# Kernel tuning notes

Hardware: AMD Instinct MI355X
Metric: run time of the kernel (lower is better)

Reference implementation:

```python
import jax, jax.numpy as jnp
import numpy as np

V = 50257   # vocab size
E = 256     # embedding_dimension
D = 8       # key_query_reduced_dimensionality
H = 8       # no_of_attention_heads
L = 16      # no_of_blocks
B = 8       # batch
T = 512     # seq len == context_size
FF = 4 * E  # MLP hidden


def setup_inputs() -> dict:
    key = jax.random.key(0)
    ks = jax.random.split(key, 12)
    rn = lambda k, s: jax.random.normal(k, s, jnp.float32) * 0.02
    return {
        'tokens': jax.random.randint(ks[0], (B, T), 0, V),
        'ideal_value': jax.random.randint(ks[1], (B, T), 0, V),
        'tok_emb': rn(ks[2], (V, E)),
        'pos_emb': rn(ks[3], (T, E)),
        'Wq': rn(ks[4], (L, H, E, D)),
        'Wk': rn(ks[5], (L, H, E, D)),
        'Wv': rn(ks[6], (L, H, E, D)),
        'Wo': rn(ks[7], (L, H * D, E)),
        'bo': jnp.zeros((L, E), jnp.float32),
        'ln1_s': jnp.ones((L, E), jnp.float32),
        'ln1_b': jnp.zeros((L, E), jnp.float32),
        'W1': rn(ks[8], (L, E, FF)),
        'b1': jnp.zeros((L, FF), jnp.float32),
        'W2': rn(ks[9], (L, FF, E)),
        'b2': jnp.zeros((L, E), jnp.float32),
        'ln2_s': jnp.ones((L, E), jnp.float32),
        'ln2_b': jnp.zeros((L, E), jnp.float32),
        'lnf_s': jnp.ones((E,), jnp.float32),
        'lnf_b': jnp.zeros((E,), jnp.float32),
        'Wf': rn(ks[10], (E, V)),
        'bf': jnp.zeros((V,), jnp.float32),
    }


def _ln(x, s, b):
    m = x.mean(-1, keepdims=True)
    v = ((x - m) ** 2).mean(-1, keepdims=True)
    return (x - m) * jax.lax.rsqrt(v + 1e-5) * s + b


def reference(tokens, ideal_value, tok_emb, pos_emb, Wq, Wk, Wv, Wo, bo,
              ln1_s, ln1_b, W1, b1, W2, b2, ln2_s, ln2_b, lnf_s, lnf_b, Wf, bf):
    Bn, Tn = tokens.shape
    x = tok_emb[tokens] + pos_emb[:Tn]                      # [B,T,E]
    # faithful mask: masked_fill where transpose(tril(R))==0 -> keep upper triangle
    keep = jnp.triu(jnp.ones((D, D), bool))
    scale = jnp.float32(E) ** 0.5

    def block(x, p):
        wq, wk, wv, wo, bo_, s1, bb1, w1, bm1, w2, bm2, s2, bb2 = p
        h = _ln(x, s1, bb1)
        Q = jnp.einsum('bte,hed->bhtd', h, wq)              # [B,H,T,D]
        K = jnp.einsum('bte,hed->bhtd', h, wk)
        Vv = jnp.einsum('bte,hed->bhtd', h, wv)
        # R = K^T @ Q : feature-by-feature [B,H,D,D] (this repo's quirky attention)
        R = jnp.einsum('bhti,bhtj->bhij', K, Q) / scale
        R = jax.nn.softmax(jnp.where(keep, R, -jnp.inf), axis=-1)
        a = jnp.einsum('bhti,bhij->bhtj', Vv, R)            # V @ R, [B,H,T,D]
        a = a.transpose(0, 2, 1, 3).reshape(x.shape[0], x.shape[1], H * D)
        x = x + a @ wo + bo_                                # dropout is identity (eval)
        h2 = _ln(x, s2, bb2)
        x = x + jax.nn.relu(h2 @ w1 + bm1) @ w2 + bm2
        return x, None

    x, _ = jax.lax.scan(block, x, (Wq, Wk, Wv, Wo, bo, ln1_s, ln1_b,
                                   W1, b1, W2, b2, ln2_s, ln2_b))
    logits = (_ln(x, lnf_s, lnf_b) @ Wf + bf).reshape(-1, V)  # [B*T, V]
    tgt = ideal_value.reshape(-1)
    logp = jax.nn.log_softmax(logits, axis=-1)
    loss = -jnp.take_along_axis(logp, tgt[:, None], axis=1).mean()
    return logits, loss
```

## Files before the change

kernel.cpp:

```cpp
#include <hip/hip_runtime.h>
#include <math.h>

#define V_SZ 50257
#define NPAD 50432
#define NCB 197

#define AS1 __attribute__((address_space(1)))
#define AS3 __attribute__((address_space(3)))

typedef short s16x8 __attribute__((ext_vector_type(8)));
typedef ushort u16x4 __attribute__((ext_vector_type(4)));
typedef float f32x4 __attribute__((ext_vector_type(4)));

__device__ __forceinline__ ushort f2bf(float x) {
    union { float f; unsigned u; } v; v.f = x;
    unsigned r = v.u + 0x7FFF + ((v.u >> 16) & 1);
    return (ushort)(r >> 16);
}
__device__ __forceinline__ float bf2f(ushort u) {
    union { unsigned u; float f; } v; v.u = ((unsigned)u) << 16; return v.f;
}

__global__ __launch_bounds__(256) void gpt_embed_ln(const int* __restrict__ tokens,
                                                    const float* __restrict__ tok_emb,
                                                    const float* __restrict__ pos_emb,
                                                    const float* __restrict__ s, const float* __restrict__ b,
                                                    float* __restrict__ x, ushort* __restrict__ hb) {
    int wave = threadIdx.x >> 6, lane = threadIdx.x & 63;
    int row = blockIdx.x * 4 + wave;
    int t = row & 511;
    int tok = tokens[row];
    float4 te = ((const float4*)(tok_emb + tok * 256))[lane];
    float4 pe = ((const float4*)(pos_emb + t * 256))[lane];
    float4 v = make_float4(te.x + pe.x, te.y + pe.y, te.z + pe.z, te.w + pe.w);
    ((float4*)(x + row * 256))[lane] = v;
    float sum = v.x + v.y + v.z + v.w;
    #pragma unroll
    for (int off = 1; off < 64; off <<= 1) sum += __shfl_xor(sum, off);
    float mean = sum * (1.0f / 256.0f);
    float dx = v.x - mean, dy = v.y - mean, dz = v.z - mean, dw = v.w - mean;
    float vs = dx * dx + dy * dy + dz * dz + dw * dw;
    #pragma unroll
    for (int off = 1; off < 64; off <<= 1) vs += __shfl_xor(vs, off);
    float rstd = rsqrtf(vs * (1.0f / 256.0f) + 1e-5f);
    float4 sv = ((const float4*)s)[lane];
    float4 bv = ((const float4*)b)[lane];
    u16x4 o;
    o[0] = f2bf(dx * rstd * sv.x + bv.x);
    o[1] = f2bf(dy * rstd * sv.y + bv.y);
    o[2] = f2bf(dz * rstd * sv.z + bv.z);
    o[3] = f2bf(dw * rstd * sv.w + bv.w);
    *(u16x4*)&hb[row * 256 + lane * 4] = o;
}

__global__ __launch_bounds__(256) void cvt_transpose(const float* __restrict__ in, ushort* __restrict__ out,
                                                     int Kd, int Nd, int n_real,
                                                     int in_stride, int out_stride) {
    __shared__ __align__(16) ushort t[64][80];
    const float* inp = in + (size_t)blockIdx.z * in_stride;
    ushort* outp = out + (size_t)blockIdx.z * out_stride;
    int n0 = blockIdx.x * 64, k0 = blockIdx.y * 64;
    int tid = threadIdx.x;
    #pragma unroll
    for (int p = 0; p < 4; p++) {
        int lk = p * 16 + (tid >> 4);
        int ln = (tid & 15) * 4;
        int k = k0 + lk, n = n0 + ln;
        const float* rowp = inp + (size_t)k * Nd;
        float v0 = 0.f, v1 = 0.f, v2 = 0.f, v3 = 0.f;
        if (n + 0 < n_real) v0 = rowp[n + 0];
        if (n + 1 < n_real) v1 = rowp[n + 1];
        if (n + 2 < n_real) v2 = rowp[n + 2];
        if (n + 3 < n_real) v3 = rowp[n + 3];
        t[ln + 0][lk] = f2bf(v0);
        t[ln + 1][lk] = f2bf(v1);
        t[ln + 2][lk] = f2bf(v2);
        t[ln + 3][lk] = f2bf(v3);
    }
    __syncthreads();
    int ln = tid >> 2, kq = (tid & 3) * 16;
    ushort* op = outp + (size_t)(n0 + ln) * Kd + k0 + kq;
    *(s16x8*)&op[0] = *(const s16x8*)&t[ln][kq];
    *(s16x8*)&op[8] = *(const s16x8*)&t[ln][kq + 8];
}

__global__ __launch_bounds__(256) void cvt_qkv(const float* __restrict__ Wq, const float* __restrict__ Wk,
                                               const float* __restrict__ Wv, ushort* __restrict__ WqkvT) {
    int l = blockIdx.x, kind = blockIdx.y;
    const float* W = (kind == 0 ? Wq : (kind == 1 ? Wk : Wv)) + l * 16384;
    ushort* out = WqkvT + (size_t)l * 65536 + kind * 64 * 256;
    int tid = threadIdx.x;
    #pragma unroll 4
    for (int it = 0; it < 64; it++) {
        int idx = it * 256 + tid;
        int row = idx >> 8, e = idx & 255;
        int h = row >> 3, d = row & 7;
        out[row * 256 + e] = f2bf(W[h * 2048 + e * 8 + d]);
    }
    if (kind == 0) {
        ushort* zp = WqkvT + (size_t)l * 65536 + 192 * 256;
        #pragma unroll 4
        for (int it = 0; it < 64; it++) zp[it * 256 + tid] = 0;
    }
}

__global__ __launch_bounds__(512, 4) void gpt_pre(const ushort* __restrict__ hb,
                                                  const ushort* __restrict__ WqkvT,
                                                  ushort* __restrict__ Vb,
                                                  float* __restrict__ Rpart) {
    __shared__ __align__(16) ushort As[16 * 64];
    __shared__ __align__(16) ushort Bs[256 * 64];
    __shared__ float kqv[16][193];
    const int tid = threadIdx.x, lane = tid & 63, wn = tid >> 6;
    const int rows0 = blockIdx.x * 16;
    const int fr = lane & 15, fkb = (lane >> 4) * 16;
    const int arow = tid >> 3, ach = tid & 7;

    f32x4 acc[2];
    acc[0] = (f32x4)0.0f; acc[1] = (f32x4)0.0f;

    s16x8 ra, rb[4];
    if (tid < 128) ra = *(const s16x8*)&hb[(size_t)(rows0 + arow) * 256 + ach * 8];
    #pragma unroll
    for (int i = 0; i < 4; i++) {
        int u = tid + i * 512, r = u >> 3, ch = u & 7;
        rb[i] = *(const s16x8*)&WqkvT[(size_t)r * 256 + ch * 8];
    }
    #pragma unroll 1
    for (int kt = 0; kt < 4; kt++) {
        if (kt) __syncthreads();
        if (tid < 128)
            *(s16x8*)&As[arow * 64 + (((ach * 16) ^ ((arow & 7) << 4)) >> 1)] = ra;
        #pragma unroll
        for (int i = 0; i < 4; i++) {
            int u = tid + i * 512, r = u >> 3, ch = u & 7;
            *(s16x8*)&Bs[r * 64 + (((ch * 16) ^ ((r & 7) << 4)) >> 1)] = rb[i];
        }
        __syncthreads();
        if (kt < 3) {
            int k0 = (kt + 1) * 64;
            if (tid < 128) ra = *(const s16x8*)&hb[(size_t)(rows0 + arow) * 256 + k0 + ach * 8];
            #pragma unroll
            for (int i = 0; i < 4; i++) {
                int u = tid + i * 512, r = u >> 3, ch = u & 7;
                rb[i] = *(const s16x8*)&WqkvT[(size_t)r * 256 + k0 + ch * 8];
            }
        }
        #pragma unroll
        for (int kk = 0; kk < 2; kk++) {
            int kbyte = kk * 64 + fkb;
            s16x8 af = *(const s16x8*)&As[fr * 64 + ((kbyte ^ ((fr & 7) << 4)) >> 1)];
            #pragma unroll
            for (int n = 0; n < 2; n++) {
                int brow = wn * 32 + n * 16 + fr;
                s16x8 bfv = *(const s16x8*)&Bs[brow * 64 + ((kbyte ^ ((brow & 7) << 4)) >> 1)];
                acc[n] = __builtin_amdgcn_mfma_f32_16x16x32_bf16(af, bfv, acc[n], 0, 0, 0);
            }
        }
    }
    #pragma unroll
    for (int n = 0; n < 2; n++) {
        int col = wn * 32 + n * 16 + fr;
        if (col < 192) {
            #pragma unroll
            for (int r = 0; r < 4; r++)
                kqv[(lane >> 4) * 4 + r][col] = acc[n][r];
        }
    }
    __syncthreads();
    #pragma unroll
    for (int i = 0; i < 2; i++) {
        int u = tid + i * 512, t = u >> 6, hd = u & 63;
        Vb[(size_t)(rows0 + t) * 64 + hd] = f2bf(kqv[t][128 + hd]);
    }
    {
        int h = tid >> 6, i2 = (tid >> 3) & 7, j = tid & 7;
        float s = 0.0f;
        #pragma unroll
        for (int t = 0; t < 16; t++)
            s += kqv[t][64 + h * 8 + i2] * kqv[t][h * 8 + j];
        int bb = rows0 >> 9, part = (rows0 >> 4) & 31;
        Rpart[(size_t)(bb * 32 + part) * 512 + tid] = s;
    }
}

__global__ __launch_bounds__(512, 4) void gpt_layer(
        const float* __restrict__ Rpart_in, const ushort* __restrict__ Vb_in,
        const ushort* __restrict__ WoT, const float* __restrict__ bo,
        const ushort* __restrict__ W1T, const float* __restrict__ b1,
        const ushort* __restrict__ W2T, const float* __restrict__ b2,
        const float* __restrict__ ls2, const float* __restrict__ lb2,
        const float* __restrict__ nls, const float* __restrict__ nlb,
        float* __restrict__ x,
        const ushort* __restrict__ WqkvT_next,
        ushort* __restrict__ Vb_out, float* __restrict__ Rpart_out,
        ushort* __restrict__ hbout, int mode) {
    __shared__ __align__(16) ushort Bs[256 * 64];
    __shared__ __align__(16) ushort ffs[16 * 1024];
    __shared__ __align__(16) ushort h2s[16 * 256];
    __shared__ __align__(16) ushort abl[16 * 64];
    __shared__ __align__(16) ushort Vl[16 * 64];
    __shared__ float Rs[512];
    __shared__ float red1[16][8], red2[16][8], mrow[16], rrow[16];

    const int tid = threadIdx.x, lane = tid & 63, wn = tid >> 6;
    const int rows0 = blockIdx.x * 16, b = rows0 >> 9;
    const int fr = lane & 15, fkb = (lane >> 4) * 16, rbase = (lane >> 4) * 4;
    int colv[2]; colv[0] = wn * 32 + fr; colv[1] = wn * 32 + 16 + fr;
    int srow_[4], sch_[4];
    #pragma unroll
    for (int i = 0; i < 4; i++) {
        int u = lane + i * 64;
        srow_[i] = wn * 32 + (u >> 3);
        sch_[i] = u & 7;
    }

    float xr[2][4];
    #pragma unroll
    for (int n = 0; n < 2; n++)
        #pragma unroll
        for (int r = 0; r < 4; r++)
            xr[n][r] = x[(size_t)(rows0 + rbase + r) * 256 + colv[n]];

    {
        const float* rp = Rpart_in + (size_t)b * 32 * 512 + tid;
        float s = 0.0f;
        #pragma unroll
        for (int p = 0; p < 32; p++) s += rp[p * 512];
        s *= (1.0f / 16.0f);
        int ii = (tid >> 3) & 7, j = tid & 7;
        float val = (j >= ii) ? s : -INFINITY;
        float m = val;
        #pragma unroll
        for (int off = 1; off < 8; off <<= 1) m = fmaxf(m, __shfl_xor(m, off, 8));
        float ex = __expf(val - m);
        float su = ex;
        #pragma unroll
        for (int off = 1; off < 8; off <<= 1) su += __shfl_xor(su, off, 8);
        Rs[tid] = ex / su;
    }
    #pragma unroll
    for (int i = 0; i < 2; i++) {
        int u = tid + i * 512, t = u >> 6, hd = u & 63;
        Vl[t * 64 + hd] = Vb_in[(size_t)(rows0 + t) * 64 + hd];
    }
    __syncthreads();
    #pragma unroll
    for (int i = 0; i < 2; i++) {
        int u = tid + i * 512, t = u >> 6, hd = u & 63, h = hd >> 3, j = hd & 7;
        float a = 0.0f;
        #pragma unroll
        for (int q = 0; q < 8; q++)
            a += bf2f(Vl[t * 64 + h * 8 + q]) * Rs[h * 64 + q * 8 + j];
        abl[t * 64 + (((hd * 2) ^ ((t & 7) << 4)) >> 1)] = f2bf(a);
    }
    s16x8 rbv[4];
    #pragma unroll
    for (int i = 0; i < 4; i++)
        rbv[i] = *(const s16x8*)&WoT[(size_t)srow_[i] * 64 + sch_[i] * 8];
    __syncthreads();
    #pragma unroll
    for (int i = 0; i < 4; i++)
        *(s16x8*)&Bs[srow_[i] * 64 + (((sch_[i] * 16) ^ ((srow_[i] & 7) << 4)) >> 1)] = rbv[i];
    f32x4 acc[2];
    acc[0] = (f32x4)0.0f; acc[1] = (f32x4)0.0f;
    __builtin_amdgcn_s_setprio(1);
    #pragma unroll
    for (int kk = 0; kk < 2; kk++) {
        int kbyte = kk * 64 + fkb;
        s16x8 af = *(const s16x8*)&abl[fr * 64 + ((kbyte ^ ((fr & 7) << 4)) >> 1)];
        #pragma unroll
        for (int n = 0; n < 2; n++) {
            int brow = wn * 32 + n * 16 + fr;
            s16x8 bfv = *(const s16x8*)&Bs[brow * 64 + ((kbyte ^ ((brow & 7) << 4)) >> 1)];
            acc[n] = __builtin_amdgcn_mfma_f32_16x16x32_bf16(af, bfv, acc[n], 0, 0, 0);
        }
    }
    __builtin_amdgcn_s_setprio(0);
    float xn[2][4];
    #pragma unroll
    for (int n = 0; n < 2; n++) {
        int col = colv[n];
        float bbv = bo[col];
        #pragma unroll
        for (int r = 0; r < 4; r++)
            xn[n][r] = acc[n][r] + bbv + xr[n][r];
    }
    #pragma unroll
    for (int r = 0; r < 4; r++) {
        float s1 = xn[0][r] + xn[1][r];
        float s2 = xn[0][r] * xn[0][r] + xn[1][r] * xn[1][r];
        #pragma unroll
        for (int off = 1; off < 16; off <<= 1) {
            s1 += __shfl_xor(s1, off);
            s2 += __shfl_xor(s2, off);
        }
        if (fr == 0) { red1[rbase + r][wn] = s1; red2[rbase + r][wn] = s2; }
    }
    __syncthreads();
    if (tid < 16) {
        float s1 = 0.f, s2 = 0.f;
        #pragma unroll
        for (int w = 0; w < 8; w++) { s1 += red1[tid][w]; s2 += red2[tid][w]; }
        float mean = s1 * (1.0f / 256.0f);
        float var = s2 * (1.0f / 256.0f) - mean * mean;
        mrow[tid] = mean;
        rrow[tid] = rsqrtf(var + 1e-5f);
    }
    __syncthreads();
    #pragma unroll
    for (int n = 0; n < 2; n++) {
        int col = colv[n];
        float lsv = ls2[col], lbv = lb2[col];
        #pragma unroll
        for (int r = 0; r < 4; r++) {
            int rl = rbase + r;
            float hv = (xn[n][r] - mrow[rl]) * rrow[rl] * lsv + lbv;
            h2s[rl * 256 + (((col * 2) ^ ((rl & 7) << 4)) >> 1)] = f2bf(hv);
        }
    }
    __syncthreads();
    #pragma unroll 1
    for (int c = 0; c < 4; c++) {
        const ushort* Bg = W1T + (size_t)c * 256 * 256;
        acc[0] = (f32x4)0.0f; acc[1] = (f32x4)0.0f;
        #pragma unroll
        for (int i = 0; i < 4; i++)
            rbv[i] = *(const s16x8*)&Bg[(size_t)srow_[i] * 256 + sch_[i] * 8];
        #pragma unroll 1
        for (int kt = 0; kt < 4; kt++) {
            #pragma unroll
            for (int i = 0; i < 4; i++)
                *(s16x8*)&Bs[srow_[i] * 64 + (((sch_[i] * 16) ^ ((srow_[i] & 7) << 4)) >> 1)] = rbv[i];
            if (kt < 3) {
                int k0 = (kt + 1) * 64;
                #pragma unroll
                for (int i = 0; i < 4; i++)
                    rbv[i] = *(const s16x8*)&Bg[(size_t)srow_[i] * 256 + k0 + sch_[i] * 8];
            }
            __builtin_amdgcn_s_setprio(1);
            #pragma unroll
            for (int kk = 0; kk < 2; kk++) {
                int kbyte = kt * 128 + kk * 64 + fkb;
                s16x8 af = *(const s16x8*)&h2s[fr * 256 + ((kbyte ^ ((fr & 7) << 4)) >> 1)];
                int kb2 = kk * 64 + fkb;
                #pragma unroll
                for (int n = 0; n < 2; n++) {
                    int brow = wn * 32 + n * 16 + fr;
                    s16x8 bfv = *(const s16x8*)&Bs[brow * 64 + ((kb2 ^ ((brow & 7) << 4)) >> 1)];
                    acc[n] = __builtin_amdgcn_mfma_f32_16x16x32_bf16(af, bfv, acc[n], 0, 0, 0);
                }
            }
            __builtin_amdgcn_s_setprio(0);
        }
        #pragma unroll
        for (int n = 0; n < 2; n++) {
            int col = c * 256 + colv[n];
            float bb1 = b1[col];
            #pragma unroll
            for (int r = 0; r < 4; r++) {
                int rl = rbase + r;
                ffs[rl * 1024 + (((col * 2) ^ ((rl & 7) << 4)) >> 1)] =
                    f2bf(fmaxf(acc[n][r] + bb1, 0.0f));
            }
        }
    }
    __syncthreads();
    f32x4 a2[2];
    a2[0] = (f32x4)0.0f; a2[1] = (f32x4)0.0f;
    #pragma unroll
    for (int i = 0; i < 4; i++)
        rbv[i] = *(const s16x8*)&W2T[(size_t)srow_[i] * 1024 + sch_[i] * 8];
    #pragma unroll 2
    for (int kt = 0; kt < 16; kt++) {
        #pragma unroll
        for (int i = 0; i < 4; i++)
            *(s16x8*)&Bs[srow_[i] * 64 + (((sch_[i] * 16) ^ ((srow_[i] & 7) << 4)) >> 1)] = rbv[i];
        if (kt < 15) {
            int k0 = (kt + 1) * 64;
            #pragma unroll
            for (int i = 0; i < 4; i++)
                rbv[i] = *(const s16x8*)&W2T[(size_t)srow_[i] * 1024 + k0 + sch_[i] * 8];
        }
        __builtin_amdgcn_s_setprio(1);
        #pragma unroll
        for (int kk = 0; kk < 2; kk++) {
            int kbyte = kt * 128 + kk * 64 + fkb;
            s16x8 af = *(const s16x8*)&ffs[fr * 1024 + ((kbyte ^ ((fr & 7) << 4)) >> 1)];
            int kb2 = kk * 64 + fkb;
            #pragma unroll
            for (int n = 0; n < 2; n++) {
                int brow = wn * 32 + n * 16 + fr;
                s16x8 bfv = *(const s16x8*)&Bs[brow * 64 + ((kb2 ^ ((brow & 7) << 4)) >> 1)];
                a2[n] = __builtin_amdgcn_mfma_f32_16x16x32_bf16(af, bfv, a2[n], 0, 0, 0);
            }
        }
        __builtin_amdgcn_s_setprio(0);
    }
    #pragma unroll
    for (int n = 0; n < 2; n++) {
        int col = colv[n];
        float bb2 = b2[col];
        #pragma unroll
        for (int r = 0; r < 4; r++) {
            float v = xn[n][r] + a2[n][r] + bb2;
            xn[n][r] = v;
            x[(size_t)(rows0 + rbase + r) * 256 + col] = v;
        }
    }
    __syncthreads();
    #pragma unroll
    for (int r = 0; r < 4; r++) {
        float s1 = xn[0][r] + xn[1][r];
        float s2 = xn[0][r] * xn[0][r] + xn[1][r] * xn[1][r];
        #pragma unroll
        for (int off = 1; off < 16; off <<= 1) {
            s1 += __shfl_xor(s1, off);
            s2 += __shfl_xor(s2, off);
        }
        if (fr == 0) { red1[rbase + r][wn] = s1; red2[rbase + r][wn] = s2; }
    }
    __syncthreads();
    if (tid < 16) {
        float s1 = 0.f, s2 = 0.f;
        #pragma unroll
        for (int w = 0; w < 8; w++) { s1 += red1[tid][w]; s2 += red2[tid][w]; }
        float mean = s1 * (1.0f / 256.0f);
        float var = s2 * (1.0f / 256.0f) - mean * mean;
        mrow[tid] = mean;
        rrow[tid] = rsqrtf(var + 1e-5f);
    }
    __syncthreads();
    #pragma unroll
    for (int n = 0; n < 2; n++) {
        int col = colv[n];
        float lsv = nls[col], lbv = nlb[col];
        #pragma unroll
        for (int r = 0; r < 4; r++) {
            int rl = rbase + r;
            float hv = (xn[n][r] - mrow[rl]) * rrow[rl] * lsv + lbv;
            ushort hu = f2bf(hv);
            h2s[rl * 256 + (((col * 2) ^ ((rl & 7) << 4)) >> 1)] = hu;
            if (mode == 0)
                hbout[(size_t)(rows0 + rl) * 256 + col] = hu;
        }
    }
    if (mode == 0) return;
    __syncthreads();

    float* kqv = (float*)ffs;
    acc[0] = (f32x4)0.0f; acc[1] = (f32x4)0.0f;
    #pragma unroll
    for (int i = 0; i < 4; i++)
        rbv[i] = *(const s16x8*)&WqkvT_next[(size_t)srow_[i] * 256 + sch_[i] * 8];
    #pragma unroll 1
    for (int kt = 0; kt < 4; kt++) {
        #pragma unroll
        for (int i = 0; i < 4; i++)
            *(s16x8*)&Bs[srow_[i] * 64 + (((sch_[i] * 16) ^ ((srow_[i] & 7) << 4)) >> 1)] = rbv[i];
        if (kt < 3) {
            int k0 = (kt + 1) * 64;
            #pragma unroll
            for (int i = 0; i < 4; i++)
                rbv[i] = *(const s16x8*)&WqkvT_next[(size_t)srow_[i] * 256 + k0 + sch_[i] * 8];
        }
        __builtin_amdgcn_s_setprio(1);
        #pragma unroll
        for (int kk = 0; kk < 2; kk++) {
            int kbyte = kt * 128 + kk * 64 + fkb;
            s16x8 af = *(const s16x8*)&h2s[fr * 256 + ((kbyte ^ ((fr & 7) << 4)) >> 1)];
            int kb2 = kk * 64 + fkb;
            #pragma unroll
            for (int n = 0; n < 2; n++) {
                int brow = wn * 32 + n * 16 + fr;
                s16x8 bfv = *(const s16x8*)&Bs[brow * 64 + ((kb2 ^ ((brow & 7) << 4)) >> 1)];
                acc[n] = __builtin_amdgcn_mfma_f32_16x16x32_bf16(af, bfv, acc[n], 0, 0, 0);
            }
        }
        __builtin_amdgcn_s_setprio(0);
    }
    __syncthreads();
    #pragma unroll
    for (int n = 0; n < 2; n++) {
        int col = wn * 32 + n * 16 + fr;
        if (col < 192) {
            #pragma unroll
            for (int r = 0; r < 4; r++)
                kqv[(rbase + r) * 193 + col] = acc[n][r];
        }
    }
    __syncthreads();
    #pragma unroll
    for (int i = 0; i < 2; i++) {
        int u = tid + i * 512, t = u >> 6, hd = u & 63;
        Vb_out[(size_t)(rows0 + t) * 64 + hd] = f2bf(kqv[t * 193 + 128 + hd]);
    }
    {
        int h = tid >> 6, i2 = (tid >> 3) & 7, j = tid & 7;
        float s = 0.0f;
        #pragma unroll
        for (int t = 0; t < 16; t++)
            s += kqv[t * 193 + 64 + h * 8 + i2] * kqv[t * 193 + h * 8 + j];
        int part = (rows0 >> 4) & 31;
        Rpart_out[(size_t)(b * 32 + part) * 512 + tid] = s;
    }
}

__global__ __launch_bounds__(512, 4) void gpt_logits_mfma(const ushort* __restrict__ hb, const ushort* __restrict__ WfT,
                                                          const float* __restrict__ bfb, float* __restrict__ out,
                                                          float2* __restrict__ lsebuf) {
    __shared__ __align__(16) ushort As[128 * 64];
    __shared__ __align__(16) ushort Bs[256 * 64];
    f32x4 acc[4][4];
    int flat = blockIdx.y * 32 + blockIdx.x;
    int nf = (flat & 7) * 788 + (flat >> 3);
    int rb = nf & 31, cb = nf >> 5;
    int row0 = rb * 128, c0 = cb * 256;
    const int tid = threadIdx.x, lane = tid & 63, wid = tid >> 6;
    const int wm = wid >> 2, wn = wid & 3;
    const int fr = lane & 15, fkb = (lane >> 4) * 16;

    #pragma unroll
    for (int m = 0; m < 4; m++)
        #pragma unroll
        for (int n = 0; n < 4; n++) acc[m][n] = (f32x4)0.0f;

    float bb[4]; int gcv[4];
    #pragma unroll
    for (int n = 0; n < 4; n++) {
        int gc = c0 + wn * 64 + n * 16 + fr;
        gcv[n] = gc;
        bb[n] = (gc < V_SZ) ? bfb[gc] : 0.0f;
    }

    const int srow = lane >> 3;
    const int sch = lane & 7;
    #pragma unroll 1
    for (int kt = 0; kt < 4; kt++) {
        if (kt) __syncthreads();
        {
            int kb = kt * 64;
            #pragma unroll
            for (int i = 0; i < 2; i++) {
                int rloc = wid * 16 + i * 8 + srow;
                int cs = sch ^ (rloc & 7);
                const ushort* gp = &hb[(size_t)(row0 + rloc) * 256 + kb + cs * 8];
                __builtin_amdgcn_global_load_lds((const AS1 void*)gp,
                                                 (AS3 void*)&As[(wid * 16 + i * 8) * 64], 16, 0, 0);
            }
            #pragma unroll
            for (int i = 0; i < 4; i++) {
                int rloc = wid * 32 + i * 8 + srow;
                int cs = sch ^ (rloc & 7);
                const ushort* gp = &WfT[(size_t)(c0 + rloc) * 256 + kb + cs * 8];
                __builtin_amdgcn_global_load_lds((const AS1 void*)gp,
                                                 (AS3 void*)&Bs[(wid * 32 + i * 8) * 64], 16, 0, 0);
            }
        }
        __syncthreads();
        #pragma unroll
        for (int kk = 0; kk < 2; kk++) {
            int kbyte = kk * 64 + fkb;
            s16x8 af[4], bfr[4];
            #pragma unroll
            for (int m = 0; m < 4; m++) {
                int arow = wm * 64 + m * 16 + fr;
                af[m] = *(const s16x8*)&As[arow * 64 + ((kbyte ^ ((arow & 7) << 4)) >> 1)];
            }
            #pragma unroll
            for (int n = 0; n < 4; n++) {
                int brow = wn * 64 + n * 16 + fr;
                bfr[n] = *(const s16x8*)&Bs[brow * 64 + ((kbyte ^ ((brow & 7) << 4)) >> 1)];
            }
            #pragma unroll
            for (int m = 0; m < 4; m++)
                #pragma unroll
                for (int n = 0; n < 4; n++)
                    acc[m][n] = __builtin_amdgcn_mfma_f32_16x16x32_bf16(af[m], bfr[n], acc[m][n], 0, 0, 0);
        }
    }
    __syncthreads();
    float2 (*red)[4] = (float2(*)[4])As;
    #pragma unroll
    for (int m = 0; m < 4; m++) {
        int rloc = wm * 64 + m * 16 + (lane >> 4) * 4;
        int gr = row0 + rloc;
        #pragma unroll
// ... 302 lines not shown
            acc1[r] += hv.x * w10 + hv.y * w11 + hv.z * w12 + hv.w * w13;
        }
    }
    if (c0 < V_SZ) {
        #pragma unroll
        for (int r = 0; r < 32; r++) out[(size_t)(row0 + r) * V_SZ + c0] = acc0[r];
    }
    if (c1 < V_SZ) {
        #pragma unroll
        for (int r = 0; r < 32; r++) out[(size_t)(row0 + r) * V_SZ + c1] = acc1[r];
    }
}

__global__ void gpt_loss(const float* __restrict__ logits, const int* __restrict__ tgt,
                         float* __restrict__ partial) {
    __shared__ float ms[256], ss[256];
    int row = blockIdx.x, tid = threadIdx.x;
    const float* lr = logits + (size_t)row * V_SZ;
    float m = -INFINITY, s = 0.0f;
    for (int c = tid; c < V_SZ; c += 256) {
        float v = lr[c];
        float nm = fmaxf(m, v);
        s = s * expf(m - nm) + expf(v - nm);
        m = nm;
    }
    ms[tid] = m; ss[tid] = s;
    __syncthreads();
    for (int off = 128; off > 0; off >>= 1) {
        if (tid < off) {
            float m2 = ms[tid + off], s2 = ss[tid + off];
            float M = fmaxf(ms[tid], m2);
            ss[tid] = ss[tid] * expf(ms[tid] - M) + s2 * expf(m2 - M);
            ms[tid] = M;
        }
        __syncthreads();
    }
    if (tid == 0) {
        float lse = ms[0] + logf(ss[0]);
        partial[row] = lse - lr[tgt[row]];
    }
}

extern "C" void kernel_launch(void* const* d_in, const int* in_sizes, int n_in,
                              void* d_out, int out_size, void* d_ws, size_t ws_size,
                              hipStream_t stream) {
    const int*   tokens  = (const int*)d_in[0];
    const int*   ideal   = (const int*)d_in[1];
    const float* tok_emb = (const float*)d_in[2];
    const float* pos_emb = (const float*)d_in[3];
    const float* Wq      = (const float*)d_in[4];
    const float* Wk      = (const float*)d_in[5];
    const float* Wv      = (const float*)d_in[6];
    const float* Wo      = (const float*)d_in[7];
    const float* bo      = (const float*)d_in[8];
    const float* ln1_s   = (const float*)d_in[9];
    const float* ln1_b   = (const float*)d_in[10];
    const float* W1      = (const float*)d_in[11];
    const float* b1      = (const float*)d_in[12];
    const float* W2      = (const float*)d_in[13];
    const float* b2      = (const float*)d_in[14];
    const float* ln2_s   = (const float*)d_in[15];
    const float* ln2_b   = (const float*)d_in[16];
    const float* lnf_s   = (const float*)d_in[17];
    const float* lnf_b   = (const float*)d_in[18];
    const float* Wf      = (const float*)d_in[19];
    const float* bf      = (const float*)d_in[20];
    float* out = (float*)d_out;

    size_t off = 0;
    char* wsc = (char*)d_ws;
    ushort* WfT   = (ushort*)(wsc + off); off += (size_t)NPAD * 256 * 2;
    ushort* W1T   = (ushort*)(wsc + off); off += (size_t)16 * 1024 * 256 * 2;
    ushort* W2T   = (ushort*)(wsc + off); off += (size_t)16 * 256 * 1024 * 2;
    ushort* WqkvT = (ushort*)(wsc + off); off += (size_t)16 * 256 * 256 * 2;
    ushort* WoT   = (ushort*)(wsc + off); off += (size_t)16 * 256 * 64 * 2;
    ushort* hb    = (ushort*)(wsc + off); off += (size_t)4096 * 256 * 2;
    ushort* Vb0   = (ushort*)(wsc + off); off += (size_t)4096 * 64 * 2;
    ushort* Vb1   = (ushort*)(wsc + off); off += (size_t)4096 * 64 * 2;
    float*  x     = (float*)(wsc + off);  off += (size_t)4096 * 256 * 4;
    float*  Rp0   = (float*)(wsc + off);  off += (size_t)8 * 32 * 512 * 4;
    float*  Rp1   = (float*)(wsc + off);  off += (size_t)8 * 32 * 512 * 4;
    float*  partial = (float*)(wsc + off); off += (size_t)4096 * 4;
    float2* lsebuf = (float2*)(wsc + off); off += (size_t)4096 * NCB * 8;
    bool big = ws_size >= off;

    if (big) {
        cvt_transpose<<<dim3(16, 4, 16), 256, 0, stream>>>(W1, W1T, 256, 1024, 1024, 262144, 262144);
        cvt_transpose<<<dim3(4, 16, 16), 256, 0, stream>>>(W2, W2T, 1024, 256, 256, 262144, 262144);
        cvt_transpose<<<dim3(4, 1, 16), 256, 0, stream>>>(Wo, WoT, 64, 256, 256, 16384, 16384);
        cvt_transpose<<<dim3(788, 4, 1), 256, 0, stream>>>(Wf, WfT, 256, V_SZ, V_SZ, 0, 0);
        cvt_qkv<<<dim3(16, 3), 256, 0, stream>>>(Wq, Wk, Wv, WqkvT);

        gpt_embed_ln<<<1024, 256, 0, stream>>>(tokens, tok_emb, pos_emb, ln1_s, ln1_b, x, hb);
        gpt_pre<<<256, 512, 0, stream>>>(hb, WqkvT, Vb0, Rp0);

        for (int l = 0; l < 16; l++) {
            const float* nls = (l < 15) ? ln1_s + (l + 1) * 256 : lnf_s;
            const float* nlb = (l < 15) ? ln1_b + (l + 1) * 256 : lnf_b;
            const float* Rin = (l & 1) ? Rp1 : Rp0;
            const ushort* Vin = (l & 1) ? Vb1 : Vb0;
            float* Rout = (l & 1) ? Rp0 : Rp1;
            ushort* Vout = (l & 1) ? Vb0 : Vb1;
            int mode = (l < 15) ? 1 : 0;
            const ushort* Wnext = WqkvT + (size_t)((l < 15) ? (l + 1) : 0) * 65536;
            gpt_layer<<<256, 512, 0, stream>>>(Rin, Vin,
                                               WoT + (size_t)l * 16384, bo + l * 256,
                                               W1T + (size_t)l * 262144, b1 + l * 1024,
                                               W2T + (size_t)l * 262144, b2 + l * 256,
                                               ln2_s + l * 256, ln2_b + l * 256,
                                               nls, nlb, x,
                                               Wnext, Vout, Rout, hb, mode);
        }

        gpt_logits_mfma<<<dim3(32, NCB), 512, 0, stream>>>(hb, WfT, bf, out, lsebuf);
        gpt_lse<<<1024, 256, 0, stream>>>(lsebuf, out, ideal, partial);
        gpt_loss_reduce<<<1, 256, 0, stream>>>(partial, out + (size_t)4096 * V_SZ);
    } else {
        float* fx  = (float*)d_ws;
        float* fh  = fx + 4096 * 256;
        float* fQ  = fh + 4096 * 256;
        float* fK  = fQ + 4096 * 64;
        float* fV  = fK + 4096 * 64;
        float* fR  = fV + 4096 * 64;
        float* fpart = fR + 64 * 64;
        gpt_embed<<<4096, 256, 0, stream>>>(tokens, tok_emb, pos_emb, fx);
        for (int l = 0; l < 16; l++) {
            gpt_ln<<<4096, 256, 0, stream>>>(fx, ln1_s + l * 256, ln1_b + l * 256, fh);
            gpt_qkv<<<512, 256, 0, stream>>>(fh, Wq + l * 16384, Wk + l * 16384, Wv + l * 16384, fQ, fK, fV);
            gpt_attn_r<<<64, 64, 0, stream>>>(fK, fQ, fR);
            gpt_attn_out<<<512, 256, 0, stream>>>(fV, fR, Wo + l * 16384, bo + l * 256, fx);
            gpt_ln<<<4096, 256, 0, stream>>>(fx, ln2_s + l * 256, ln2_b + l * 256, fh);
            gpt_mlp<<<512, 256, 0, stream>>>(fh, W1 + l * 262144, b1 + l * 1024, W2 + l * 262144, b2 + l * 256, fx);
        }
        gpt_ln<<<4096, 256, 0, stream>>>(fx, lnf_s, lnf_b, fh);
        dim3 lg(99, 128);
        gpt_logits<<<lg, 256, 0, stream>>>(fh, Wf, bf, out);
        gpt_loss<<<4096, 256, 0, stream>>>(out, ideal, fpart);
        gpt_loss_reduce<<<1, 256, 0, stream>>>(fpart, out + (size_t)4096 * V_SZ);
    }
}
```

Before: 910.0 us.

## Fuse all transformer layers into one persistent kernel with grid barriers

Replaces the sixteen per-layer launches with one persistent kernel that loops over layers. Each 16-row block keeps its residual stream in registers instead of reloading and storing x every layer. Layers are separated by a global atomic-counter barrier, since the attention R reduction needs every block of a batch. This removes launch gaps and global traffic for x. The cost is a spin-wait barrier, which relies on all 256 blocks being resident at once.

```diff
diff --git a/kernel.cpp b/kernel.cpp
--- a/kernel.cpp
+++ b/kernel.cpp
@@ -19,6 +19,10 @@
 }
 __device__ __forceinline__ float bf2f(ushort u) {
     union { unsigned u; float f; } v; v.u = ((unsigned)u) << 16; return v.f;
+}
+
+__global__ void gpt_zero(unsigned* __restrict__ c) {
+    if (threadIdx.x < 16) c[threadIdx.x] = 0;
 }
 
 __global__ __launch_bounds__(256) void gpt_embed_ln(const int* __restrict__ tokens,
@@ -184,17 +188,18 @@
     }
 }
 
-__global__ __launch_bounds__(512, 4) void gpt_layer(
-        const float* __restrict__ Rpart_in, const ushort* __restrict__ Vb_in,
-        const ushort* __restrict__ WoT, const float* __restrict__ bo,
-        const ushort* __restrict__ W1T, const float* __restrict__ b1,
-        const ushort* __restrict__ W2T, const float* __restrict__ b2,
-        const float* __restrict__ ls2, const float* __restrict__ lb2,
-        const float* __restrict__ nls, const float* __restrict__ nlb,
-        float* __restrict__ x,
-        const ushort* __restrict__ WqkvT_next,
-        ushort* __restrict__ Vb_out, float* __restrict__ Rpart_out,
-        ushort* __restrict__ hbout, int mode) {
+__global__ __launch_bounds__(512, 4) void gpt_layers_all(
+        float* __restrict__ Rp0, ushort* __restrict__ Vb0,
+        float* __restrict__ Rp1, ushort* __restrict__ Vb1,
+        const ushort* __restrict__ WoT_a, const float* __restrict__ bo_a,
+        const ushort* __restrict__ W1T_a, const float* __restrict__ b1_a,
+        const ushort* __restrict__ W2T_a, const float* __restrict__ b2_a,
+        const float* __restrict__ ln2s_a, const float* __restrict__ ln2b_a,
+        const float* __restrict__ ln1s_a, const float* __restrict__ ln1b_a,
+        const float* __restrict__ lnf_s, const float* __restrict__ lnf_b,
+        const ushort* __restrict__ WqkvT_a,
+        const float* __restrict__ x0, ushort* __restrict__ hbout,
+        unsigned* __restrict__ cnts) {
     __shared__ __align__(16) ushort Bs[256 * 64];
     __shared__ __align__(16) ushort ffs[16 * 1024];
     __shared__ __align__(16) ushort h2s[16 * 256];
@@ -215,118 +220,258 @@
         sch_[i] = u & 7;
     }
 
-    float xr[2][4];
+    float xc[2][4];
     #pragma unroll
     for (int n = 0; n < 2; n++)
         #pragma unroll
         for (int r = 0; r < 4; r++)
-            xr[n][r] = x[(size_t)(rows0 + rbase + r) * 256 + colv[n]];
-
-    {
-        const float* rp = Rpart_in + (size_t)b * 32 * 512 + tid;
-        float s = 0.0f;
-        #pragma unroll
-        for (int p = 0; p < 32; p++) s += rp[p * 512];
-        s *= (1.0f / 16.0f);
-        int ii = (tid >> 3) & 7, j = tid & 7;
-        float val = (j >= ii) ? s : -INFINITY;
-        float m = val;
-        #pragma unroll
-        for (int off = 1; off < 8; off <<= 1) m = fmaxf(m, __shfl_xor(m, off, 8));
-        float ex = __expf(val - m);
-        float su = ex;
-        #pragma unroll
-        for (int off = 1; off < 8; off <<= 1) su += __shfl_xor(su, off, 8);
-        Rs[tid] = ex / su;
-    }
-    #pragma unroll
-    for (int i = 0; i < 2; i++) {
-        int u = tid + i * 512, t = u >> 6, hd = u & 63;
-        Vl[t * 64 + hd] = Vb_in[(size_t)(rows0 + t) * 64 + hd];
-    }
-    __syncthreads();
-    #pragma unroll
-    for (int i = 0; i < 2; i++) {
-        int u = tid + i * 512, t = u >> 6, hd = u & 63, h = hd >> 3, j = hd & 7;
-        float a = 0.0f;
-        #pragma unroll
-        for (int q = 0; q < 8; q++)
-            a += bf2f(Vl[t * 64 + h * 8 + q]) * Rs[h * 64 + q * 8 + j];
-        abl[t * 64 + (((hd * 2) ^ ((t & 7) << 4)) >> 1)] = f2bf(a);
-    }
-    s16x8 rbv[4];
-    #pragma unroll
-    for (int i = 0; i < 4; i++)
-        rbv[i] = *(const s16x8*)&WoT[(size_t)srow_[i] * 64 + sch_[i] * 8];
-    __syncthreads();
-    #pragma unroll
-    for (int i = 0; i < 4; i++)
-        *(s16x8*)&Bs[srow_[i] * 64 + (((sch_[i] * 16) ^ ((srow_[i] & 7) << 4)) >> 1)] = rbv[i];
-    f32x4 acc[2];
-    acc[0] = (f32x4)0.0f; acc[1] = (f32x4)0.0f;
-    __builtin_amdgcn_s_setprio(1);
-    #pragma unroll
-    for (int kk = 0; kk < 2; kk++) {
-        int kbyte = kk * 64 + fkb;
-        s16x8 af = *(const s16x8*)&abl[fr * 64 + ((kbyte ^ ((fr & 7) << 4)) >> 1)];
+            xc[n][r] = x0[(size_t)(rows0 + rbase + r) * 256 + colv[n]];
+
+    #pragma unroll 1
+    for (int l = 0; l < 16; l++) {
+        const float*  Rpart_in  = (l & 1) ? Rp1 : Rp0;
+        const ushort* Vb_in     = (l & 1) ? Vb1 : Vb0;
+        float*        Rpart_out = (l & 1) ? Rp0 : Rp1;
+        ushort*       Vb_out    = (l & 1) ? Vb0 : Vb1;
+        const ushort* WoT = WoT_a + (size_t)l * 16384;
+        const float*  bo  = bo_a + l * 256;
+        const ushort* W1T = W1T_a + (size_t)l * 262144;
+        const float*  b1  = b1_a + l * 1024;
+        const ushort* W2T = W2T_a + (size_t)l * 262144;
+        const float*  b2  = b2_a + l * 256;
+        const float*  ls2 = ln2s_a + l * 256;
+        const float*  lb2 = ln2b_a + l * 256;
+        const int mode = (l < 15);
+        const float* nls = mode ? ln1s_a + (l + 1) * 256 : lnf_s;
+        const float* nlb = mode ? ln1b_a + (l + 1) * 256 : lnf_b;
+        const ushort* WqkvT_next = WqkvT_a + (size_t)(mode ? (l + 1) : 0) * 65536;
+
+        {
+            const float* rp = Rpart_in + (size_t)b * 32 * 512 + tid;
+            float s = 0.0f;
+            #pragma unroll
+            for (int p = 0; p < 32; p++) s += rp[p * 512];
+            s *= (1.0f / 16.0f);
+            int ii = (tid >> 3) & 7, j = tid & 7;
+            float val = (j >= ii) ? s : -INFINITY;
+            float m = val;
+            #pragma unroll
+            for (int off = 1; off < 8; off <<= 1) m = fmaxf(m, __shfl_xor(m, off, 8));
+            float ex = __expf(val - m);
+            float su = ex;
+            #pragma unroll
+            for (int off = 1; off < 8; off <<= 1) su += __shfl_xor(su, off, 8);
+            Rs[tid] = ex / su;
+        }
+        #pragma unroll
+        for (int i = 0; i < 2; i++) {
+            int u = tid + i * 512, t = u >> 6, hd = u & 63;
+            Vl[t * 64 + hd] = Vb_in[(size_t)(rows0 + t) * 64 + hd];
+        }
+        __syncthreads();
+        #pragma unroll
+        for (int i = 0; i < 2; i++) {
+            int u = tid + i * 512, t = u >> 6, hd = u & 63, h = hd >> 3, j = hd & 7;
+            float a = 0.0f;
+            #pragma unroll
+            for (int q = 0; q < 8; q++)
+                a += bf2f(Vl[t * 64 + h * 8 + q]) * Rs[h * 64 + q * 8 + j];
+            abl[t * 64 + (((hd * 2) ^ ((t & 7) << 4)) >> 1)] = f2bf(a);
+        }
+        s16x8 rbv[4];
+        #pragma unroll
+        for (int i = 0; i < 4; i++)
+            rbv[i] = *(const s16x8*)&WoT[(size_t)srow_[i] * 64 + sch_[i] * 8];
+        __syncthreads();
+        #pragma unroll
+        for (int i = 0; i < 4; i++)
+            *(s16x8*)&Bs[srow_[i] * 64 + (((sch_[i] * 16) ^ ((srow_[i] & 7) << 4)) >> 1)] = rbv[i];
+        f32x4 acc[2];
+        acc[0] = (f32x4)0.0f; acc[1] = (f32x4)0.0f;
+        __builtin_amdgcn_s_setprio(1);
+        #pragma unroll
+        for (int kk = 0; kk < 2; kk++) {
+            int kbyte = kk * 64 + fkb;
+            s16x8 af = *(const s16x8*)&abl[fr * 64 + ((kbyte ^ ((fr & 7) << 4)) >> 1)];
+            #pragma unroll
+            for (int n = 0; n < 2; n++) {
+                int brow = wn * 32 + n * 16 + fr;
+                s16x8 bfv = *(const s16x8*)&Bs[brow * 64 + ((kbyte ^ ((brow & 7) << 4)) >> 1)];
+                acc[n] = __builtin_amdgcn_mfma_f32_16x16x32_bf16(af, bfv, acc[n], 0, 0, 0);
+            }
+        }
+        __builtin_amdgcn_s_setprio(0);
+        float xn[2][4];
         #pragma unroll
         for (int n = 0; n < 2; n++) {
-            int brow = wn * 32 + n * 16 + fr;
-            s16x8 bfv = *(const s16x8*)&Bs[brow * 64 + ((kbyte ^ ((brow & 7) << 4)) >> 1)];
-            acc[n] = __builtin_amdgcn_mfma_f32_16x16x32_bf16(af, bfv, acc[n], 0, 0, 0);
-        }
-    }
-    __builtin_amdgcn_s_setprio(0);
-    float xn[2][4];
-    #pragma unroll
-    for (int n = 0; n < 2; n++) {
-        int col = colv[n];
-        float bbv = bo[col];
-        #pragma unroll
-        for (int r = 0; r < 4; r++)
-            xn[n][r] = acc[n][r] + bbv + xr[n][r];
-    }
-    #pragma unroll
-    for (int r = 0; r < 4; r++) {
-        float s1 = xn[0][r] + xn[1][r];
-        float s2 = xn[0][r] * xn[0][r] + xn[1][r] * xn[1][r];
-        #pragma unroll
-        for (int off = 1; off < 16; off <<= 1) {
-            s1 += __shfl_xor(s1, off);
-            s2 += __shfl_xor(s2, off);
-        }
-        if (fr == 0) { red1[rbase + r][wn] = s1; red2[rbase + r][wn] = s2; }
-    }
-    __syncthreads();
-    if (tid < 16) {
-        float s1 = 0.f, s2 = 0.f;
-        #pragma unroll
-        for (int w = 0; w < 8; w++) { s1 += red1[tid][w]; s2 += red2[tid][w]; }
-        float mean = s1 * (1.0f / 256.0f);
-        float var = s2 * (1.0f / 256.0f) - mean * mean;
-        mrow[tid] = mean;
-        rrow[tid] = rsqrtf(var + 1e-5f);
-    }
-    __syncthreads();
-    #pragma unroll
-    for (int n = 0; n < 2; n++) {
-        int col = colv[n];
-        float lsv = ls2[col], lbv = lb2[col];
+            float bbv = bo[colv[n]];
+            #pragma unroll
+            for (int r = 0; r < 4; r++)
+                xn[n][r] = acc[n][r] + bbv + xc[n][r];
+        }
         #pragma unroll
         for (int r = 0; r < 4; r++) {
-            int rl = rbase + r;
-            float hv = (xn[n][r] - mrow[rl]) * rrow[rl] * lsv + lbv;
-            h2s[rl * 256 + (((col * 2) ^ ((rl & 7) << 4)) >> 1)] = f2bf(hv);
-        }
-    }
-    __syncthreads();
-    #pragma unroll 1
-    for (int c = 0; c < 4; c++) {
-        const ushort* Bg = W1T + (size_t)c * 256 * 256;
+            float s1 = xn[0][r] + xn[1][r];
+            float s2 = xn[0][r] * xn[0][r] + xn[1][r] * xn[1][r];
+            #pragma unroll
+            for (int off = 1; off < 16; off <<= 1) {
+                s1 += __shfl_xor(s1, off);
+                s2 += __shfl_xor(s2, off);
+            }
+            if (fr == 0) { red1[rbase + r][wn] = s1; red2[rbase + r][wn] = s2; }
+        }
+        __syncthreads();
+        if (tid < 16) {
+            float s1 = 0.f, s2 = 0.f;
+            #pragma unroll
+            for (int w = 0; w < 8; w++) { s1 += red1[tid][w]; s2 += red2[tid][w]; }
+            float mean = s1 * (1.0f / 256.0f);
+            float var = s2 * (1.0f / 256.0f) - mean * mean;
+            mrow[tid] = mean;
+            rrow[tid] = rsqrtf(var + 1e-5f);
+        }
+        __syncthreads();
+        #pragma unroll
+        for (int n = 0; n < 2; n++) {
+            int col = colv[n];
+            float lsv = ls2[col], lbv = lb2[col];
+            #pragma unroll
+            for (int r = 0; r < 4; r++) {
+                int rl = rbase + r;
+                float hv = (xn[n][r] - mrow[rl]) * rrow[rl] * lsv + lbv;
+                h2s[rl * 256 + (((col * 2) ^ ((rl & 7) << 4)) >> 1)] = f2bf(hv);
+            }
+        }
+        __syncthreads();
+        #pragma unroll 1
+        for (int c = 0; c < 4; c++) {
+            const ushort* Bg = W1T + (size_t)c * 256 * 256;
+            acc[0] = (f32x4)0.0f; acc[1] = (f32x4)0.0f;
+            #pragma unroll
+            for (int i = 0; i < 4; i++)
+                rbv[i] = *(const s16x8*)&Bg[(size_t)srow_[i] * 256 + sch_[i] * 8];
+            #pragma unroll 1
+            for (int kt = 0; kt < 4; kt++) {
+                #pragma unroll
+                for (int i = 0; i < 4; i++)
+                    *(s16x8*)&Bs[srow_[i] * 64 + (((sch_[i] * 16) ^ ((srow_[i] & 7) << 4)) >> 1)] = rbv[i];
+                if (kt < 3) {
+                    int k0 = (kt + 1) * 64;
+                    #pragma unroll
+                    for (int i = 0; i < 4; i++)
+                        rbv[i] = *(const s16x8*)&Bg[(size_t)srow_[i] * 256 + k0 + sch_[i] * 8];
+                }
+                __builtin_amdgcn_s_setprio(1);
+                #pragma unroll
+                for (int kk = 0; kk < 2; kk++) {
+                    int kbyte = kt * 128 + kk * 64 + fkb;
+                    s16x8 af = *(const s16x8*)&h2s[fr * 256 + ((kbyte ^ ((fr & 7) << 4)) >> 1)];
+                    int kb2 = kk * 64 + fkb;
+                    #pragma unroll
+                    for (int n = 0; n < 2; n++) {
+                        int brow = wn * 32 + n * 16 + fr;
+                        s16x8 bfv = *(const s16x8*)&Bs[brow * 64 + ((kb2 ^ ((brow & 7) << 4)) >> 1)];
+                        acc[n] = __builtin_amdgcn_mfma_f32_16x16x32_bf16(af, bfv, acc[n], 0, 0, 0);
+                    }
+                }
+                __builtin_amdgcn_s_setprio(0);
+            }
+            #pragma unroll
+            for (int n = 0; n < 2; n++) {
+                int col = c * 256 + colv[n];
+                float bb1 = b1[col];
+                #pragma unroll
+                for (int r = 0; r < 4; r++) {
+                    int rl = rbase + r;
+                    ffs[rl * 1024 + (((col * 2) ^ ((rl & 7) << 4)) >> 1)] =
+                        f2bf(fmaxf(acc[n][r] + bb1, 0.0f));
+                }
+            }
+        }
+        __syncthreads();
+        f32x4 a2[2];
+        a2[0] = (f32x4)0.0f; a2[1] = (f32x4)0.0f;
+        #pragma unroll
+        for (int i = 0; i < 4; i++)
+            rbv[i] = *(const s16x8*)&W2T[(size_t)srow_[i] * 1024 + sch_[i] * 8];
+        #pragma unroll 2
+        for (int kt = 0; kt < 16; kt++) {
+            #pragma unroll
+            for (int i = 0; i < 4; i++)
+                *(s16x8*)&Bs[srow_[i] * 64 + (((sch_[i] * 16) ^ ((srow_[i] & 7) << 4)) >> 1)] = rbv[i];
+            if (kt < 15) {
+                int k0 = (kt + 1) * 64;
+                #pragma unroll
+                for (int i = 0; i < 4; i++)
+                    rbv[i] = *(const s16x8*)&W2T[(size_t)srow_[i] * 1024 + k0 + sch_[i] * 8];
+            }
+            __builtin_amdgcn_s_setprio(1);
+            #pragma unroll
+            for (int kk = 0; kk < 2; kk++) {
+                int kbyte = kt * 128 + kk * 64 + fkb;
+                s16x8 af = *(const s16x8*)&ffs[fr * 1024 + ((kbyte ^ ((fr & 7) << 4)) >> 1)];
+                int kb2 = kk * 64 + fkb;
+                #pragma unroll
+                for (int n = 0; n < 2; n++) {
+                    int brow = wn * 32 + n * 16 + fr;
+                    s16x8 bfv = *(const s16x8*)&Bs[brow * 64 + ((kb2 ^ ((brow & 7) << 4)) >> 1)];
+                    a2[n] = __builtin_amdgcn_mfma_f32_16x16x32_bf16(af, bfv, a2[n], 0, 0, 0);
+                }
+            }
+            __builtin_amdgcn_s_setprio(0);
+        }
+        #pragma unroll
+        for (int n = 0; n < 2; n++) {
+            float bb2 = b2[colv[n]];
+            #pragma unroll
+            for (int r = 0; r < 4; r++)
+                xc[n][r] = xn[n][r] + a2[n][r] + bb2;
+        }
+        __syncthreads();
+        #pragma unroll
+        for (int r = 0; r < 4; r++) {
+            float s1 = xc[0][r] + xc[1][r];
+            float s2 = xc[0][r] * xc[0][r] + xc[1][r] * xc[1][r];
+            #pragma unroll
+            for (int off = 1; off < 16; off <<= 1) {
+                s1 += __shfl_xor(s1, off);
+                s2 += __shfl_xor(s2, off);
+            }
+            if (fr == 0) { red1[rbase + r][wn] = s1; red2[rbase + r][wn] = s2; }
+        }
+        __syncthreads();
+        if (tid < 16) {
+            float s1 = 0.f, s2 = 0.f;
+            #pragma unroll
+            for (int w = 0; w < 8; w++) { s1 += red1[tid][w]; s2 += red2[tid][w]; }
+            float mean = s1 * (1.0f / 256.0f);
+            float var = s2 * (1.0f / 256.0f) - mean * mean;
+            mrow[tid] = mean;
+            rrow[tid] = rsqrtf(var + 1e-5f);
+        }
+        __syncthreads();
+        #pragma unroll
+        for (int n = 0; n < 2; n++) {
+            int col = colv[n];
+            float lsv = nls[col], lbv = nlb[col];
+            #pragma unroll
+            for (int r = 0; r < 4; r++) {
+                int rl = rbase + r;
+                float hv = (xc[n][r] - mrow[rl]) * rrow[rl] * lsv + lbv;
+                ushort hu = f2bf(hv);
+                h2s[rl * 256 + (((col * 2) ^ ((rl & 7) << 4)) >> 1)] = hu;
+                if (!mode)
+                    hbout[(size_t)(rows0 + rl) * 256 + col] = hu;
+            }
+        }
+        if (!mode) break;
+        __syncthreads();
+
+        float* kqv = (float*)ffs;
         acc[0] = (f32x4)0.0f; acc[1] = (f32x4)0.0f;
         #pragma unroll
         for (int i = 0; i < 4; i++)
-            rbv[i] = *(const s16x8*)&Bg[(size_t)srow_[i] * 256 + sch_[i] * 8];
+            rbv[i] = *(const s16x8*)&WqkvT_next[(size_t)srow_[i] * 256 + sch_[i] * 8];
         #pragma unroll 1
         for (int kt = 0; kt < 4; kt++) {
             #pragma unroll
@@ -336,7 +481,7 @@
                 int k0 = (kt + 1) * 64;
                 #pragma unroll
                 for (int i = 0; i < 4; i++)
-                    rbv[i] = *(const s16x8*)&Bg[(size_t)srow_[i] * 256 + k0 + sch_[i] * 8];
+                    rbv[i] = *(const s16x8*)&WqkvT_next[(size_t)srow_[i] * 256 + k0 + sch_[i] * 8];
             }
             __builtin_amdgcn_s_setprio(1);
             #pragma unroll
@@ -353,156 +498,40 @@
             }
             __builtin_amdgcn_s_setprio(0);
         }
+        __syncthreads();
         #pragma unroll
         for (int n = 0; n < 2; n++) {
-            int col = c * 256 + colv[n];
-            float bb1 = b1[col];
-            #pragma unroll
-            for (int r = 0; r < 4; r++) {
-                int rl = rbase + r;
-                ffs[rl * 1024 + (((col * 2) ^ ((rl & 7) << 4)) >> 1)] =
-                    f2bf(fmaxf(acc[n][r] + bb1, 0.0f));
-            }
-        }
-    }
-    __syncthreads();
-    f32x4 a2[2];
-    a2[0] = (f32x4)0.0f; a2[1] = (f32x4)0.0f;
-    #pragma unroll
-    for (int i = 0; i < 4; i++)
-        rbv[i] = *(const s16x8*)&W2T[(size_t)srow_[i] * 1024 + sch_[i] * 8];
-    #pragma unroll 2
-    for (int kt = 0; kt < 16; kt++) {
-        #pragma unroll
-        for (int i = 0; i < 4; i++)
-            *(s16x8*)&Bs[srow_[i] * 64 + (((sch_[i] * 16) ^ ((srow_[i] & 7) << 4)) >> 1)] = rbv[i];
-        if (kt < 15) {
-            int k0 = (kt + 1) * 64;
-            #pragma unroll
-            for (int i = 0; i < 4; i++)
-                rbv[i] = *(const s16x8*)&W2T[(size_t)srow_[i] * 1024 + k0 + sch_[i] * 8];
-        }
-        __builtin_amdgcn_s_setprio(1);
-        #pragma unroll
-        for (int kk = 0; kk < 2; kk++) {
-            int kbyte = kt * 128 + kk * 64 + fkb;
-            s16x8 af = *(const s16x8*)&ffs[fr * 1024 + ((kbyte ^ ((fr & 7) << 4)) >> 1)];
-            int kb2 = kk * 64 + fkb;
-            #pragma unroll
-            for (int n = 0; n < 2; n++) {
-                int brow = wn * 32 + n * 16 + fr;
-                s16x8 bfv = *(const s16x8*)&Bs[brow * 64 + ((kb2 ^ ((brow & 7) << 4)) >> 1)];
-                a2[n] = __builtin_amdgcn_mfma_f32_16x16x32_bf16(af, bfv, a2[n], 0, 0, 0);
-            }
-        }
-        __builtin_amdgcn_s_setprio(0);
-    }
-    #pragma unroll
-    for (int n = 0; n < 2; n++) {
-        int col = colv[n];
-        float bb2 = b2[col];
-        #pragma unroll
-        for (int r = 0; r < 4; r++) {
-            float v = xn[n][r] + a2[n][r] + bb2;
-            xn[n][r] = v;
-            x[(size_t)(rows0 + rbase + r) * 256 + col] = v;
-        }
-    }
-    __syncthreads();
-    #pragma unroll
-    for (int r = 0; r < 4; r++) {
-        float s1 = xn[0][r] + xn[1][r];
-        float s2 = xn[0][r] * xn[0][r] + xn[1][r] * xn[1][r];
-        #pragma unroll
-        for (int off = 1; off < 16; off <<= 1) {
-            s1 += __shfl_xor(s1, off);
-            s2 += __shfl_xor(s2, off);
-        }
-        if (fr == 0) { red1[rbase + r][wn] = s1; red2[rbase + r][wn] = s2; }
-    }
-    __syncthreads();
-    if (tid < 16) {
-        float s1 = 0.f, s2 = 0.f;
-        #pragma unroll
-        for (int w = 0; w < 8; w++) { s1 += red1[tid][w]; s2 += red2[tid][w]; }
-        float mean = s1 * (1.0f / 256.0f);
-        float var = s2 * (1.0f / 256.0f) - mean * mean;
-        mrow[tid] = mean;
-        rrow[tid] = rsqrtf(var + 1e-5f);
-    }
-    __syncthreads();
-    #pragma unroll
-    for (int n = 0; n < 2; n++) {
-        int col = colv[n];
-        float lsv = nls[col], lbv = nlb[col];
-        #pragma unroll
-        for (int r = 0; r < 4; r++) {
-            int rl = rbase + r;
-            float hv = (xn[n][r] - mrow[rl]) * rrow[rl] * lsv + lbv;
-            ushort hu = f2bf(hv);
-            h2s[rl * 256 + (((col * 2) ^ ((rl & 7) << 4)) >> 1)] = hu;
-            if (mode == 0)
-                hbout[(size_t)(rows0 + rl) * 256 + col] = hu;
-        }
-    }
-    if (mode == 0) return;
-    __syncthreads();
-
-    float* kqv = (float*)ffs;
-    acc[0] = (f32x4)0.0f; acc[1] = (f32x4)0.0f;
-    #pragma unroll
-    for (int i = 0; i < 4; i++)
-        rbv[i] = *(const s16x8*)&WqkvT_next[(size_t)srow_[i] * 256 + sch_[i] * 8];
-    #pragma unroll 1
-    for (int kt = 0; kt < 4; kt++) {
-        #pragma unroll
-        for (int i = 0; i < 4; i++)
-            *(s16x8*)&Bs[srow_[i] * 64 + (((sch_[i] * 16) ^ ((srow_[i] & 7) << 4)) >> 1)] = rbv[i];
-        if (kt < 3) {
-            int k0 = (kt + 1) * 64;
-            #pragma unroll
-            for (int i = 0; i < 4; i++)
-                rbv[i] = *(const s16x8*)&WqkvT_next[(size_t)srow_[i] * 256 + k0 + sch_[i] * 8];
-        }
-        __builtin_amdgcn_s_setprio(1);
-        #pragma unroll
-        for (int kk = 0; kk < 2; kk++) {
-            int kbyte = kt * 128 + kk * 64 + fkb;
-            s16x8 af = *(const s16x8*)&h2s[fr * 256 + ((kbyte ^ ((fr & 7) << 4)) >> 1)];
-            int kb2 = kk * 64 + fkb;
-            #pragma unroll
-            for (int n = 0; n < 2; n++) {
-                int brow = wn * 32 + n * 16 + fr;
-                s16x8 bfv = *(const s16x8*)&Bs[brow * 64 + ((kb2 ^ ((brow & 7) << 4)) >> 1)];
-                acc[n] = __builtin_amdgcn_mfma_f32_16x16x32_bf16(af, bfv, acc[n], 0, 0, 0);
-            }
-        }
-        __builtin_amdgcn_s_setprio(0);
-    }
-    __syncthreads();
-    #pragma unroll
-    for (int n = 0; n < 2; n++) {
-        int col = wn * 32 + n * 16 + fr;
-        if (col < 192) {
-            #pragma unroll
-            for (int r = 0; r < 4; r++)
-                kqv[(rbase + r) * 193 + col] = acc[n][r];
-        }
-    }
-    __syncthreads();
-    #pragma unroll
-    for (int i = 0; i < 2; i++) {
-        int u = tid + i * 512, t = u >> 6, hd = u & 63;
-        Vb_out[(size_t)(rows0 + t) * 64 + hd] = f2bf(kqv[t * 193 + 128 + hd]);
-    }
-    {
-        int h = tid >> 6, i2 = (tid >> 3) & 7, j = tid & 7;
-        float s = 0.0f;
-        #pragma unroll
-        for (int t = 0; t < 16; t++)
-            s += kqv[t * 193 + 64 + h * 8 + i2] * kqv[t * 193 + h * 8 + j];
-        int part = (rows0 >> 4) & 31;
-        Rpart_out[(size_t)(b * 32 + part) * 512 + tid] = s;
+            int col = wn * 32 + n * 16 + fr;
+            if (col < 192) {
+                #pragma unroll
+                for (int r = 0; r < 4; r++)
+                    kqv[(rbase + r) * 193 + col] = acc[n][r];
+            }
+        }
+        __syncthreads();
+        #pragma unroll
+        for (int i = 0; i < 2; i++) {
+            int u = tid + i * 512, t = u >> 6, hd = u & 63;
+            Vb_out[(size_t)(rows0 + t) * 64 + hd] = f2bf(kqv[t * 193 + 128 + hd]);
+        }
+        {
+            int h = tid >> 6, i2 = (tid >> 3) & 7, j = tid & 7;
+            float s = 0.0f;
+            #pragma unroll
+            for (int t = 0; t < 16; t++)
+                s += kqv[t * 193 + 64 + h * 8 + i2] * kqv[t * 193 + h * 8 + j];
+            int part = (rows0 >> 4) & 31;
+            Rpart_out[(size_t)(b * 32 + part) * 512 + tid] = s;
+        }
+        __syncthreads();
+        if (tid == 0) {
+            __threadfence();
+            __hip_atomic_fetch_add(&cnts[l], 1u, __ATOMIC_ACQ_REL, __HIP_MEMORY_SCOPE_AGENT);
+            while (__hip_atomic_load(&cnts[l], __ATOMIC_ACQUIRE, __HIP_MEMORY_SCOPE_AGENT) < 256u) {
+                __builtin_amdgcn_s_sleep(2);
+            }
+        }
+        __syncthreads();
     }
 }
 
@@ -971,9 +1000,11 @@
     float*  Rp1   = (float*)(wsc + off);  off += (size_t)8 * 32 * 512 * 4;
     float*  partial = (float*)(wsc + off); off += (size_t)4096 * 4;
     float2* lsebuf = (float2*)(wsc + off); off += (size_t)4096 * NCB * 8;
+    unsigned* cnts = (unsigned*)(wsc + off); off += 16 * sizeof(unsigned);
     bool big = ws_size >= off;
 
     if (big) {
+        gpt_zero<<<1, 64, 0, stream>>>(cnts);
         cvt_transpose<<<dim3(16, 4, 16), 256, 0, stream>>>(W1, W1T, 256, 1024, 1024, 262144, 262144);
         cvt_transpose<<<dim3(4, 16, 16), 256, 0, stream>>>(W2, W2T, 1024, 256, 256, 262144, 262144);
         cvt_transpose<<<dim3(4, 1, 16), 256, 0, stream>>>(Wo, WoT, 64, 256, 256, 16384, 16384);
@@ -983,23 +1014,11 @@
         gpt_embed_ln<<<1024, 256, 0, stream>>>(tokens, tok_emb, pos_emb, ln1_s, ln1_b, x, hb);
         gpt_pre<<<256, 512, 0, stream>>>(hb, WqkvT, Vb0, Rp0);
 
-        for (int l = 0; l < 16; l++) {
-            const float* nls = (l < 15) ? ln1_s + (l + 1) * 256 : lnf_s;
-            const float* nlb = (l < 15) ? ln1_b + (l + 1) * 256 : lnf_b;
-            const float* Rin = (l & 1) ? Rp1 : Rp0;
-            const ushort* Vin = (l & 1) ? Vb1 : Vb0;
-            float* Rout = (l & 1) ? Rp0 : Rp1;
-            ushort* Vout = (l & 1) ? Vb0 : Vb1;
-            int mode = (l < 15) ? 1 : 0;
-            const ushort* Wnext = WqkvT + (size_t)((l < 15) ? (l + 1) : 0) * 65536;
-            gpt_layer<<<256, 512, 0, stream>>>(Rin, Vin,
-                                               WoT + (size_t)l * 16384, bo + l * 256,
-                                               W1T + (size_t)l * 262144, b1 + l * 1024,
-                                               W2T + (size_t)l * 262144, b2 + l * 256,
-                                               ln2_s + l * 256, ln2_b + l * 256,
-                                               nls, nlb, x,
-                                               Wnext, Vout, Rout, hb, mode);
-        }
+        gpt_layers_all<<<256, 512, 0, stream>>>(Rp0, Vb0, Rp1, Vb1,
+                                                WoT, bo, W1T, b1, W2T, b2,
+                                                ln2_s, ln2_b, ln1_s, ln1_b,
+                                                lnf_s, lnf_b, WqkvT,
+                                                x, hb, cnts);
 
         gpt_logits_mfma<<<dim3(32, NCB), 512, 0, stream>>>(hb, WfT, bf, out, lsebuf);
         gpt_lse<<<1024, 256, 0, stream>>>(lsebuf, out, ideal, partial);
```

Result: slower. 1.285 ms (+41.2%).
